# Kernel tuning notes

Hardware: AMD Instinct MI355X
Metric: run time of the kernel (lower is better)

Reference implementation:

```python
import jax, jax.numpy as jnp
import numpy as np

H, D = 16, 64  # heads, d_head
ROPE_BASE = 10000.0


def _rotate_half(x):
    # '... (d r) -> ... d r' with r=2, unbind, cat(-x2, x1)
    xs = x.reshape(*x.shape[:-1], D // 2, 2)
    x1, x2 = xs[..., 0], xs[..., 1]
    return jnp.concatenate([-x2, x1], axis=-1)


def _rope_sin_cos(n):
    inv_freq = 1.0 / (ROPE_BASE ** (jnp.arange(0, D, 2, dtype=jnp.float32) / D))  # [D/2]
    f = jnp.arange(n, dtype=jnp.float32)[:, None] * inv_freq                      # [n, D/2]
    emb = jnp.concatenate([f, f], axis=-1)                                        # [n, D]
    # cache = cat(sin(emb), cos(emb)); apply slices sin=[:D], cos=[D:]
    return jnp.sin(emb), jnp.cos(emb)


def setup_inputs() -> dict:
    key = jax.random.key(0)
    ks = jax.random.split(key, 5)
    B, N, E = 2, 2048, 1024
    C = H * D
    s = 0.02
    return {
        "x": jax.random.normal(ks[0], (B, N, E), jnp.float32),
        "Wq": jax.random.normal(ks[1], (C, E), jnp.float32) * s,
        "bq": jnp.zeros((C,), jnp.float32),
        "Wk": jax.random.normal(ks[2], (C, E), jnp.float32) * s,
        "bk": jnp.zeros((C,), jnp.float32),
        "Wv": jax.random.normal(ks[3], (C, E), jnp.float32) * s,
        "bv": jnp.zeros((C,), jnp.float32),
        "Wo": jax.random.normal(ks[4], (E, C), jnp.float32) * s,
        "bo": jnp.zeros((E,), jnp.float32),
    }


def reference(x, Wq, bq, Wk, bk, Wv, bv, Wo, bo):
    B, N, E = x.shape

    def proj(W, b):  # [B,N,E] -> [B,H,N,D]
        y = x @ W.T + b
        return y.reshape(B, N, H, D).transpose(0, 2, 1, 3)

    q, k, v = proj(Wq, bq), proj(Wk, bk), proj(Wv, bv)

    sin, cos = _rope_sin_cos(N)  # each [N, D], broadcast over [B,H,N,D]
    q = q * cos + _rotate_half(q) * sin
    k = k * cos + _rotate_half(k) * sin

    scale = 1.0 / jnp.sqrt(jnp.float32(D))
    scores = jnp.einsum('bhqd,bhkd->bhqk', q, k) * scale  # [B,H,N,N]
    causal = jnp.tril(jnp.ones((N, N), dtype=bool))
    scores = jnp.where(causal, scores, jnp.float32(-jnp.inf))
    probs = jax.nn.softmax(scores, axis=-1)
    out = jnp.einsum('bhqk,bhkd->bhqd', probs, v)
    out = out.transpose(0, 2, 1, 3).reshape(B, N, H * D)
    return out @ Wo.T + bo
```

## Files before the change

kernel.cpp:

```cpp
#include <hip/hip_runtime.h>
#include <hip/hip_bf16.h>
#include <cstdint>
#include <cstddef>

using bf16x8 = __attribute__((ext_vector_type(8))) __bf16;
using f32x4  = __attribute__((ext_vector_type(4))) float;

__device__ __forceinline__ float b2f(unsigned short u) {
  union { unsigned u; float f; } x; x.u = ((unsigned)u) << 16; return x.f;
}
__device__ __forceinline__ unsigned short f2b(float f) {
  union { float f; unsigned u; } x; x.f = f;
  unsigned r = x.u + 0x7fffu + ((x.u >> 16) & 1u);
  return (unsigned short)(r >> 16);
}
__device__ __forceinline__ unsigned short f2b_trunc(float f) {
  union { float f; unsigned u; } x; x.f = f;
  return (unsigned short)(x.u >> 16);
}

__device__ __forceinline__ void gload_lds16(const void* g, void* l) {
  __builtin_amdgcn_global_load_lds(
      (const __attribute__((address_space(1))) void*)g,
      (__attribute__((address_space(3))) void*)l, 16, 0, 0);
}

__device__ __forceinline__ bf16x8 ldfrag(const unsigned short* p) {
  return *reinterpret_cast<const bf16x8*>(p);
}

__global__ __launch_bounds__(256) void prep_kernel(const float* __restrict__ x,
                                                   const float* __restrict__ Wq,
                                                   const float* __restrict__ Wk,
                                                   const float* __restrict__ Wv,
                                                   const float* __restrict__ Wo,
                                                   unsigned short* __restrict__ xb,
                                                   unsigned short* __restrict__ wqkv,
                                                   unsigned short* __restrict__ wob,
                                                   float* __restrict__ st,
                                                   float* __restrict__ ct) {
  const int gid = blockIdx.x * 256 + threadIdx.x;
  if (gid < 65536) {
    const int n = gid >> 5, j = gid & 31;
    const float inv = powf(10000.0f, -(float)j * (1.0f / 32.0f));
    const float ang = (float)n * inv;
    st[gid] = sinf(ang);
    ct[gid] = cosf(ang);
  }
  const int XW = 1048576;
  const int WW = 262144;
#pragma unroll
  for (int it = 0; it < 4; ++it) {
    const int i = gid + it * 524288;
    const float* s; unsigned short* d; int j;
    if (i < XW)                { s = x;  d = xb;              j = i; }
    else if (i < XW + WW)      { s = Wq; d = wqkv;            j = i - XW; }
    else if (i < XW + 2 * WW)  { s = Wk; d = wqkv + 1048576;  j = i - XW - WW; }
    else if (i < XW + 3 * WW)  { s = Wv; d = wqkv + 2097152;  j = i - XW - 2 * WW; }
    else                       { s = Wo; d = wob;             j = i - XW - 3 * WW; }
    float4 v = reinterpret_cast<const float4*>(s)[j];
    ushort4 o;
    o.x = f2b(v.x); o.y = f2b(v.y); o.z = f2b(v.z); o.w = f2b(v.w);
    reinterpret_cast<ushort4*>(d)[j] = o;
  }
}

__global__ __launch_bounds__(512) void gemm256(const unsigned short* __restrict__ A,
                                               const unsigned short* __restrict__ B,
                                               unsigned short* __restrict__ Qo,
                                               unsigned short* __restrict__ Ko,
                                               unsigned short* __restrict__ Vt,
                                               const float* __restrict__ st,
                                               const float* __restrict__ ct,
                                               const float* __restrict__ bq,
                                               const float* __restrict__ bk,
                                               const float* __restrict__ bv,
                                               int M, int N, int K, int TN) {
  extern __shared__ __align__(16) unsigned short sm[];
  const int tid = threadIdx.x, lane = tid & 63, wave = tid >> 6;
  const int lr = lane & 15, lk = lane >> 4;
  const int wr = wave >> 2, wc = wave & 3;

  int wg = (int)blockIdx.x;
  const int cpx = (int)gridDim.x >> 3;
  wg = (wg & 7) * cpx + (wg >> 3);
  const int bn = (wg % TN) * 192, bm = (wg / TN) * 256;

  const int srow = wave * 8 + (lane >> 3);
  const int scol = (((lane & 7) * 16) ^ (((lane >> 3) & 7) << 4)) >> 1;
  const unsigned short* Ag = A + (size_t)(bm + srow) * K + scol;
  const unsigned short* Bg = B + (size_t)(bn + srow) * K + scol;

  auto issueA = [&](int kt, int nb, int i) {
    gload_lds16(Ag + (size_t)(i * 64) * K + (size_t)kt * 64,
                sm + nb * 28672 + wave * 512 + i * 4096);
  };
  auto issueB = [&](int kt, int nb, int i) {
    gload_lds16(Bg + (size_t)(i * 64) * K + (size_t)kt * 64,
                sm + nb * 28672 + 16384 + wave * 512 + i * 4096);
  };

  f32x4 acc[8][3] = {};
  const int swz = (lr & 7) << 4;
  const int NT = K / 64;

#pragma unroll
  for (int i = 0; i < 3; ++i) issueB(0, 0, i);
#pragma unroll
  for (int i = 0; i < 4; ++i) issueA(0, 0, i);
  asm volatile("s_waitcnt vmcnt(0)" ::: "memory");
  __builtin_amdgcn_s_barrier();

  for (int kt = 0; kt < NT; ++kt) {
    const int cur = kt & 1, nb = cur ^ 1;
    const bool pf = (kt + 1 < NT);

    const unsigned short* Ab = sm + cur * 28672 + wr * 8192;
    const unsigned short* Bb = sm + cur * 28672 + 16384;

    bf16x8 b[3][2];
#pragma unroll
    for (int n = 0; n < 3; ++n)
#pragma unroll
      for (int kk = 0; kk < 2; ++kk)
        b[n][kk] = ldfrag(&Bb[(wc * 48 + n * 16 + lr) * 64 + (((kk * 64 + lk * 16) ^ swz) >> 1)]);

#pragma unroll
    for (int q = 0; q < 4; ++q) {
      if (q == 2) {
        if (pf) asm volatile("s_waitcnt vmcnt(4)" ::: "memory");
        else    asm volatile("s_waitcnt vmcnt(0)" ::: "memory");
        __builtin_amdgcn_s_barrier();
      }
      if (pf) {
        if (q == 0)      { issueB(kt + 1, nb, 0); issueB(kt + 1, nb, 1); }
        else if (q == 1) { issueB(kt + 1, nb, 2); issueA(kt + 1, nb, 0); }
        else if (q == 2) { issueA(kt + 1, nb, 1); issueA(kt + 1, nb, 2); }
        else             { issueA(kt + 1, nb, 3); }
      }
      bf16x8 a[2][2];
#pragma unroll
      for (int m = 0; m < 2; ++m)
#pragma unroll
        for (int kk = 0; kk < 2; ++kk)
          a[m][kk] = ldfrag(&Ab[((q * 2 + m) * 16 + lr) * 64 + (((kk * 64 + lk * 16) ^ swz) >> 1)]);
      __builtin_amdgcn_s_barrier();
      __builtin_amdgcn_s_setprio(1);
#pragma unroll
      for (int kk = 0; kk < 2; ++kk)
#pragma unroll
        for (int m = 0; m < 2; ++m)
#pragma unroll
          for (int n = 0; n < 3; ++n)
            acc[q * 2 + m][n] =
                __builtin_amdgcn_mfma_f32_16x16x32_bf16(a[m][kk], b[n][kk], acc[q * 2 + m][n], 0, 0, 0);
      __builtin_amdgcn_s_setprio(0);
      if (q < 3) __builtin_amdgcn_s_barrier();
    }

    if (pf) {
      asm volatile("s_waitcnt vmcnt(1)" ::: "memory");
      __builtin_amdgcn_s_barrier();
    }
  }

  __syncthreads();

  const int btok = bm >> 11;
  const int ntok0 = bm & 2047;

#pragma unroll
  for (int n = 0; n < 3; ++n) {
    const int col = bn + wc * 48 + n * 16 + lr;
    if (col >= 2048) {
      const int vcol = col - 2048;
      const float bvv = bv[vcol];
      const int h = vcol >> 6, d = vcol & 63;
      unsigned short* vrow = Vt + ((size_t)((btok * 16 + h) * 64 + d)) * 2048;
#pragma unroll
      for (int mu = 0; mu < 4; ++mu) {
        uint4 w;
        w.x = (unsigned)f2b(acc[2 * mu][n][0] + bvv)     | ((unsigned)f2b(acc[2 * mu][n][1] + bvv) << 16);
        w.y = (unsigned)f2b(acc[2 * mu][n][2] + bvv)     | ((unsigned)f2b(acc[2 * mu][n][3] + bvv) << 16);
        w.z = (unsigned)f2b(acc[2 * mu + 1][n][0] + bvv) | ((unsigned)f2b(acc[2 * mu + 1][n][1] + bvv) << 16);
        w.w = (unsigned)f2b(acc[2 * mu + 1][n][2] + bvv) | ((unsigned)f2b(acc[2 * mu + 1][n][3] + bvv) << 16);
        const int ncol = ntok0 + wr * 128 + mu * 32 + 8 * lk;
        *reinterpret_cast<uint4*>(vrow + ncol) = w;
      }
    } else {
      const float bvv = (col < 1024) ? bq[col] : bk[col & 1023];
      const int lcol = wc * 48 + n * 16 + lr;
#pragma unroll
      for (int m = 0; m < 8; ++m)
#pragma unroll
        for (int r = 0; r < 4; ++r) {
          const int lrow = wr * 128 + m * 16 + lk * 4 + r;
          const int g2 = (lcol >> 3) ^ (lrow & 7);
          sm[lrow * 192 + (g2 << 3) + (lcol & 7)] = f2b(acc[m][n][r] + bvv);
        }
    }
  }
  __syncthreads();

  const int nqk = min(3, max(0, (2048 - bn) >> 6));
  for (int t = tid; t < 256 * nqk; t += 512) {
    const int hh = t >> 8, row = t & 255;
    const int ntok = ntok0 + row;
    const int col0 = bn + hh * 64;
    const bool isq = col0 < 1024;
    const int h = (col0 & 1023) >> 6;
    const float* ctp = ct + ntok * 32;
    const float* stp = st + ntok * 32;
    unsigned short xr[64];
#pragma unroll
    for (int i = 0; i < 8; ++i) {
      const int g = (hh * 8 + i) ^ (row & 7);
      *reinterpret_cast<int4*>(&xr[i * 8]) =
          *reinterpret_cast<const int4*>(&sm[row * 192 + g * 8]);
    }
    unsigned short out[64];
#pragma unroll
    for (int i = 0; i < 32; ++i) {
      const float c = ctp[i], s = stp[i];
      float o1 = b2f(xr[i]) * c - b2f(xr[2 * i + 1]) * s;
      float o2 = b2f(xr[32 + i]) * c + b2f(xr[2 * i]) * s;
      if (isq) { o1 *= 0.18033688f; o2 *= 0.18033688f; }
      out[i] = f2b(o1);
      out[32 + i] = f2b(o2);
    }
    unsigned short* dst =
        (isq ? Qo : Ko) + ((size_t)((btok * 16 + h) * 2048 + ntok)) * 64;
#pragma unroll
    for (int i = 0; i < 8; ++i)
      *reinterpret_cast<int4*>(dst + i * 8) =
          *reinterpret_cast<const int4*>(&out[i * 8]);
  }
}

template <int OUTF32>
__global__ __launch_bounds__(256) void gemm_bt(const unsigned short* __restrict__ A,
                                               const unsigned short* __restrict__ B,
                                               void* __restrict__ C,
                                               const float* __restrict__ bias,
                                               int M, int N, int K) {
  __shared__ __align__(16) unsigned short As[128 * 32];
  __shared__ __align__(16) unsigned short Bs[128 * 32];
  const int tid = threadIdx.x;
  const int lane = tid & 63, wave = tid >> 6;
  const int wr = wave >> 1, wc = wave & 1;
  const int bm = blockIdx.y * 128, bn = blockIdx.x * 128;
  const int lr = lane & 15, lk = lane >> 4;
  f32x4 acc[4][4] = {};

  for (int k0 = 0; k0 < K; k0 += 32) {
#pragma unroll
    for (int i = 0; i < 2; ++i) {
      int idx = i * 256 + tid;
      int row = idx >> 2, c8 = (idx & 3) * 8;
      gload_lds16(A + (size_t)(bm + row) * K + k0 + c8, &As[(i * 256 + wave * 64) * 8]);
      gload_lds16(B + (size_t)(bn + row) * K + k0 + c8, &Bs[(i * 256 + wave * 64) * 8]);
    }
    __syncthreads();
    bf16x8 af[4], bfr[4];
#pragma unroll
    for (int mi = 0; mi < 4; ++mi)
      af[mi] = ldfrag(&As[(wr * 64 + mi * 16 + lr) * 32 + lk * 8]);
#pragma unroll
    for (int ni = 0; ni < 4; ++ni)
      bfr[ni] = ldfrag(&Bs[(wc * 64 + ni * 16 + lr) * 32 + lk * 8]);
#pragma unroll
    for (int mi = 0; mi < 4; ++mi)
#pragma unroll
      for (int ni = 0; ni < 4; ++ni)
        acc[mi][ni] = __builtin_amdgcn_mfma_f32_16x16x32_bf16(af[mi], bfr[ni], acc[mi][ni], 0, 0, 0);
    __syncthreads();
  }

#pragma unroll
  for (int mi = 0; mi < 4; ++mi) {
#pragma unroll
    for (int ni = 0; ni < 4; ++ni) {
      int col = bn + wc * 64 + ni * 16 + lr;
      float bv = bias ? bias[col] : 0.0f;
#pragma unroll
      for (int r = 0; r < 4; ++r) {
        int row = bm + wr * 64 + mi * 16 + lk * 4 + r;
        float v = acc[mi][ni][r] + bv;
        if (OUTF32)
          reinterpret_cast<float*>(C)[(size_t)row * N + col] = v;
        else
          reinterpret_cast<unsigned short*>(C)[(size_t)row * N + col] = f2b(v);
      }
    }
  }
}

__global__ __launch_bounds__(512) void flash_kernel(const unsigned short* __restrict__ Q,
                                                    const unsigned short* __restrict__ Kb,
                                                    const unsigned short* __restrict__ Vt,
                                                    unsigned short* __restrict__ Out, int N) {
  extern __shared__ __align__(16) unsigned short smem[];
  unsigned short* KsB = smem;
  unsigned short* VsB = smem + 16384;

  const int tid = threadIdx.x;
  const int lane = tid & 63, wave = tid >> 6;
  const int lr = lane & 15, lk = lane >> 4;
  const int bh = blockIdx.x;
  const int x = blockIdx.y;
  const int qtA = x, qtB = 15 - x;
  const int ntA = x + 1;
  const unsigned short* Qh = Q + (size_t)bh * N * 64;
  const unsigned short* Kh = Kb + (size_t)bh * N * 64;
  const unsigned short* Vh = Vt + (size_t)bh * 64 * N;

  const int wrowA = qtA * 128 + wave * 16;
  const int wrowB = qtB * 128 + wave * 16;

  const int kr = tid >> 3;
  const int kcb = ((tid & 7) * 16) ^ ((kr & 7) << 4);
  const unsigned short* Kg0 = Kh + (size_t)kr * 64 + (kcb >> 1);
  const int vr = tid >> 4;
  const int vcb = ((tid & 15) * 16) ^ ((vr & 7) << 4);
  const unsigned short* Vg0 = Vh + (size_t)vr * N + (vcb >> 1);

  auto stage = [&](int buf, int tk) {
    const unsigned short* kp = Kg0 + (size_t)tk * 8192;
    const unsigned short* vp = Vg0 + (size_t)tk * 128;
    unsigned short* kl = KsB + buf * 8192 + wave * 512;
    unsigned short* vl = VsB + buf * 8192 + wave * 512;
    gload_lds16(kp, kl);
    gload_lds16(kp + 4096, kl + 4096);
    gload_lds16(vp, vl);
    gload_lds16(vp + (size_t)32 * N, vl + 4096);
  };

  stage(0, 0);

  bf16x8 qA0 = ldfrag(&Qh[(size_t)(wrowA + lr) * 64 + lk * 8]);
  bf16x8 qA1 = ldfrag(&Qh[(size_t)(wrowA + lr) * 64 + 32 + lk * 8]);
  bf16x8 qB0 = ldfrag(&Qh[(size_t)(wrowB + lr) * 64 + lk * 8]);
  bf16x8 qB1 = ldfrag(&Qh[(size_t)(wrowB + lr) * 64 + 32 + lk * 8]);

  bf16x8 ones;
  {
    union { unsigned short u; __bf16 b; } one; one.u = 0x3F80;
#pragma unroll
    for (int j = 0; j < 8; ++j) ones[j] = one.b;
  }

  const float NEG = -1e30f;
  f32x4 oacc[4] = {};
  f32x4 lacc = {};
  float m_run = NEG;

  auto compute_phase = [&](int buf, bf16x8 q0, bf16x8 q1, bool diag) {
    const unsigned short* Ksb = KsB + buf * 8192;
    const unsigned short* Vsb = VsB + buf * 8192;
    f32x4 s[8];
#pragma unroll
    for (int ni = 0; ni < 8; ++ni) s[ni] = f32x4{0.f, 0.f, 0.f, 0.f};
    __builtin_amdgcn_s_setprio(1);
#pragma unroll
    for (int ni = 0; ni < 8; ++ni) {
      const int R = ni * 16 + lr;
      const int sw = (R & 7) << 4;
      bf16x8 kf0 = ldfrag(&Ksb[R * 64 + (((lk * 16) ^ sw) >> 1)]);
      bf16x8 kf1 = ldfrag(&Ksb[R * 64 + (((64 + lk * 16) ^ sw) >> 1)]);
      s[ni] = __builtin_amdgcn_mfma_f32_16x16x32_bf16(kf0, q0, s[ni], 0, 0, 0);
      s[ni] = __builtin_amdgcn_mfma_f32_16x16x32_bf16(kf1, q1, s[ni], 0, 0, 0);
    }
    __builtin_amdgcn_s_setprio(0);

    if (diag) {
      const int ql = wave * 16 + lr;
#pragma unroll
      for (int ni = 0; ni < 8; ++ni)
#pragma unroll
        for (int r = 0; r < 4; ++r)
          if (ni * 16 + lk * 4 + r > ql) s[ni][r] = NEG;
    }

    float mx = s[0][0];
#pragma unroll
    for (int ni = 0; ni < 8; ++ni)
#pragma unroll
      for (int r = 0; r < 4; ++r)
        if (ni || r) mx = fmaxf(mx, s[ni][r]);
    mx = fmaxf(mx, __shfl_xor(mx, 16, 64));
    mx = fmaxf(mx, __shfl_xor(mx, 32, 64));

    if (!__all(mx - m_run <= 8.0f)) {
      float nm = fmaxf(m_run, mx);
      float alpha = __builtin_amdgcn_exp2f(m_run - nm);
      m_run = nm;
#pragma unroll
      for (int ni = 0; ni < 4; ++ni) oacc[ni] *= alpha;
      lacc *= alpha;
    }

    unsigned pk[8][2];
#pragma unroll
    for (int ni = 0; ni < 8; ++ni) {
      float p0 = __builtin_amdgcn_exp2f(s[ni][0] - m_run);
      float p1 = __builtin_amdgcn_exp2f(s[ni][1] - m_run);
      float p2 = __builtin_amdgcn_exp2f(s[ni][2] - m_run);
      float p3 = __builtin_amdgcn_exp2f(s[ni][3] - m_run);
      pk[ni][0] = (unsigned)f2b_trunc(p0) | ((unsigned)f2b_trunc(p1) << 16);
      pk[ni][1] = (unsigned)f2b_trunc(p2) | ((unsigned)f2b_trunc(p3) << 16);
    }

    __builtin_amdgcn_s_setprio(1);
#pragma unroll
    for (int c = 0; c < 4; ++c) {
      union { unsigned u[4]; bf16x8 v; } pb;
      pb.u[0] = pk[2 * c][0];
      pb.u[1] = pk[2 * c][1];
      pb.u[2] = pk[2 * c + 1][0];
      pb.u[3] = pk[2 * c + 1][1];
      lacc = __builtin_amdgcn_mfma_f32_16x16x32_bf16(ones, pb.v, lacc, 0, 0, 0);
      const int cb = c * 64 + lk * 16;
#pragma unroll
      for (int ni = 0; ni < 4; ++ni) {
        const int RV = ni * 16 + lr;
        bf16x8 vf = ldfrag(&Vsb[RV * 128 + ((cb ^ ((RV & 7) << 4)) >> 1)]);
        oacc[ni] = __builtin_amdgcn_mfma_f32_16x16x32_bf16(vf, pb.v, oacc[ni], 0, 0, 0);
      }
    }
    __builtin_amdgcn_s_setprio(0);
  };

  const int b = bh >> 4, h = bh & 15;
  auto epilogue = [&](int wrow0) {
    const float rl = 1.0f / lacc[0];
    const int q = wrow0 + lr;
#pragma unroll
    for (int ni = 0; ni < 4; ++ni) {
      uint2 w;
      w.x = (unsigned)f2b(oacc[ni][0] * rl) | ((unsigned)f2b(oacc[ni][1] * rl) << 16);
      w.y = (unsigned)f2b(oacc[ni][2] * rl) | ((unsigned)f2b(oacc[ni][3] * rl) << 16);
      *reinterpret_cast<uint2*>(
          &Out[((size_t)(b * N + q)) * 1024 + h * 64 + ni * 16 + lk * 4]) = w;
    }
  };

  __syncthreads();

  int buf = 0;
  for (int p = 0; p < 17; ++p) {
    if (p + 1 < 17) {
      int tk2 = (p + 1 < ntA) ? (p + 1) : (p + 1 - ntA);
      stage(buf ^ 1, tk2);
    }
    if (p == ntA) {
      epilogue(wrowA);
#pragma unroll
      for (int ni = 0; ni < 4; ++ni) oacc[ni] = f32x4{0.f, 0.f, 0.f, 0.f};
      lacc = f32x4{0.f, 0.f, 0.f, 0.f};
      m_run = NEG;
    }
    if (p < ntA) compute_phase(buf, qA0, qA1, p == ntA - 1);
    else         compute_phase(buf, qB0, qB1, p == 16);
    __syncthreads();
    buf ^= 1;
  }
  epilogue(wrowB);
}

extern "C" void kernel_launch(void* const* d_in, const int* in_sizes, int n_in,
                              void* d_out, int out_size, void* d_ws, size_t ws_size,
                              hipStream_t stream) {
  const int B = 2, N = 2048, E = 1024, C = 1024, NC = 3072;
  const int M = B * N;

  const float* x  = (const float*)d_in[0];
  const float* Wq = (const float*)d_in[1];
  const float* bq = (const float*)d_in[2];
  const float* Wk = (const float*)d_in[3];
  const float* bk = (const float*)d_in[4];
  const float* Wv = (const float*)d_in[5];
  const float* bv = (const float*)d_in[6];
  const float* Wo = (const float*)d_in[7];
  const float* bo = (const float*)d_in[8];

  char* w = (char*)d_ws;
  size_t off = 0;
  auto alloc = [&](size_t bytes) {
    void* p = w + off;
    off += (bytes + 255) & ~(size_t)255;
    return p;
  };
  unsigned short* xb    = (unsigned short*)alloc((size_t)M * E * 2);
  unsigned short* wqkv  = (unsigned short*)alloc((size_t)NC * E * 2);
  unsigned short* wob   = (unsigned short*)alloc((size_t)E * C * 2);
  unsigned short* qb    = (unsigned short*)alloc((size_t)B * 16 * N * 64 * 2);
  unsigned short* kb    = (unsigned short*)alloc((size_t)B * 16 * N * 64 * 2);
  unsigned short* vt    = (unsigned short*)alloc((size_t)B * 16 * 64 * N * 2);
  unsigned short* attnb = (unsigned short*)alloc((size_t)M * C * 2);
  float* sin_t = (float*)alloc((size_t)N * 32 * 4);
  float* cos_t = (float*)alloc((size_t)N * 32 * 4);

  prep_kernel<<<2048, 256, 0, stream>>>(x, Wq, Wk, Wv, Wo, xb, wqkv, wob, sin_t, cos_t);

  static const int GEMM_LDS = 114688;
  hipFuncSetAttribute(reinterpret_cast<const void*>(gemm256),
                      hipFuncAttributeMaxDynamicSharedMemorySize, GEMM_LDS);
  gemm256<<<dim3((NC / 192) * (M / 256)), 512, GEMM_LDS, stream>>>(
      xb, wqkv, qb, kb, vt, sin_t, cos_t, bq, bk, bv, M, NC, E, NC / 192);

  static const int FLASH_LDS = 65536;
  hipFuncSetAttribute(reinterpret_cast<const void*>(flash_kernel),
                      hipFuncAttributeMaxDynamicSharedMemorySize, FLASH_LDS);
  flash_kernel<<<dim3(B * 16, 8), 512, FLASH_LDS, stream>>>(qb, kb, vt, attnb, N);

  gemm_bt<1><<<dim3(E / 128, M / 128), 256, 0, stream>>>(attnb, wob, d_out, bo, M, E, C);
}
```

Before: 109.9 us.

## Double-buffer output projection GEMM with swizzled LDS and BK=64

Replaces the simple single-buffered output-projection GEMM with a version that prefetches the next 64-wide K tile into a second LDS buffer while computing the current one. It adds an XOR swizzle to the LDS layout to reduce bank conflicts on fragment loads, and raises wave priority around the MFMA bursts. This aims to hide global load latency and halve the barrier count per K. In exchange it uses 64KB of dynamic LDS, which may reduce occupancy.

```diff
diff --git a/kernel.cpp b/kernel.cpp
--- a/kernel.cpp
+++ b/kernel.cpp
@@ -237,59 +237,87 @@
   }
 }
 
-template <int OUTF32>
-__global__ __launch_bounds__(256) void gemm_bt(const unsigned short* __restrict__ A,
-                                               const unsigned short* __restrict__ B,
-                                               void* __restrict__ C,
-                                               const float* __restrict__ bias,
-                                               int M, int N, int K) {
-  __shared__ __align__(16) unsigned short As[128 * 32];
-  __shared__ __align__(16) unsigned short Bs[128 * 32];
-  const int tid = threadIdx.x;
-  const int lane = tid & 63, wave = tid >> 6;
+__global__ __launch_bounds__(256) void gemm_out(const unsigned short* __restrict__ A,
+                                                const unsigned short* __restrict__ B,
+                                                float* __restrict__ C,
+                                                const float* __restrict__ bias,
+                                                int M, int N, int K) {
+  extern __shared__ __align__(16) unsigned short sm[];
+  const int tid = threadIdx.x, lane = tid & 63, wave = tid >> 6;
+  const int lr = lane & 15, lk = lane >> 4;
   const int wr = wave >> 1, wc = wave & 1;
   const int bm = blockIdx.y * 128, bn = blockIdx.x * 128;
-  const int lr = lane & 15, lk = lane >> 4;
+
+  const int srow = tid >> 3;
+  const int scol = (((tid & 7) * 16) ^ ((srow & 7) << 4)) >> 1;
+  const unsigned short* Ag = A + (size_t)(bm + srow) * K + scol;
+  const unsigned short* Bg = B + (size_t)(bn + srow) * K + scol;
+
+  auto stage = [&](int kt, int nb) {
+    const size_t ko = (size_t)kt * 64;
+    unsigned short* base = sm + nb * 16384 + wave * 512;
+#pragma unroll
+    for (int i = 0; i < 4; ++i)
+      gload_lds16(Ag + (size_t)(i * 32) * K + ko, base + i * 2048);
+#pragma unroll
+    for (int i = 0; i < 4; ++i)
+      gload_lds16(Bg + (size_t)(i * 32) * K + ko, base + 8192 + i * 2048);
+  };
+
   f32x4 acc[4][4] = {};
-
-  for (int k0 = 0; k0 < K; k0 += 32) {
-#pragma unroll
-    for (int i = 0; i < 2; ++i) {
-      int idx = i * 256 + tid;
-      int row = idx >> 2, c8 = (idx & 3) * 8;
-      gload_lds16(A + (size_t)(bm + row) * K + k0 + c8, &As[(i * 256 + wave * 64) * 8]);
-      gload_lds16(B + (size_t)(bn + row) * K + k0 + c8, &Bs[(i * 256 + wave * 64) * 8]);
-    }
-    __syncthreads();
-    bf16x8 af[4], bfr[4];
-#pragma unroll
-    for (int mi = 0; mi < 4; ++mi)
-      af[mi] = ldfrag(&As[(wr * 64 + mi * 16 + lr) * 32 + lk * 8]);
-#pragma unroll
-    for (int ni = 0; ni < 4; ++ni)
-      bfr[ni] = ldfrag(&Bs[(wc * 64 + ni * 16 + lr) * 32 + lk * 8]);
-#pragma unroll
-    for (int mi = 0; mi < 4; ++mi)
-#pragma unroll
-      for (int ni = 0; ni < 4; ++ni)
-        acc[mi][ni] = __builtin_amdgcn_mfma_f32_16x16x32_bf16(af[mi], bfr[ni], acc[mi][ni], 0, 0, 0);
-    __syncthreads();
-  }
-
-#pragma unroll
-  for (int mi = 0; mi < 4; ++mi) {
-#pragma unroll
-    for (int ni = 0; ni < 4; ++ni) {
-      int col = bn + wc * 64 + ni * 16 + lr;
-      float bv = bias ? bias[col] : 0.0f;
+  const int swz = (lr & 7) << 4;
+  const int NT = K / 64;
+
+  stage(0, 0);
+  asm volatile("s_waitcnt vmcnt(0)" ::: "memory");
+  __builtin_amdgcn_s_barrier();
+
+  for (int kt = 0; kt < NT; ++kt) {
+    const int cur = kt & 1;
+    const bool pf = (kt + 1 < NT);
+    if (pf) stage(kt + 1, cur ^ 1);
+
+    const unsigned short* Ab = sm + cur * 16384 + (size_t)wr * 64 * 64;
+    const unsigned short* Bb = sm + cur * 16384 + 8192 + (size_t)wc * 64 * 64;
+
+    bf16x8 b[4][2];
+#pragma unroll
+    for (int n = 0; n < 4; ++n)
+#pragma unroll
+      for (int kk = 0; kk < 2; ++kk)
+        b[n][kk] = ldfrag(&Bb[(n * 16 + lr) * 64 + (((kk * 64 + lk * 16) ^ swz) >> 1)]);
+
+#pragma unroll
+    for (int m = 0; m < 4; ++m) {
+      bf16x8 a[2];
+#pragma unroll
+      for (int kk = 0; kk < 2; ++kk)
+        a[kk] = ldfrag(&Ab[(m * 16 + lr) * 64 + (((kk * 64 + lk * 16) ^ swz) >> 1)]);
+      __builtin_amdgcn_s_setprio(1);
+#pragma unroll
+      for (int kk = 0; kk < 2; ++kk)
+#pragma unroll
+        for (int n = 0; n < 4; ++n)
+          acc[m][n] = __builtin_amdgcn_mfma_f32_16x16x32_bf16(a[kk], b[n][kk], acc[m][n], 0, 0, 0);
+      __builtin_amdgcn_s_setprio(0);
+    }
+
+    if (pf) {
+      asm volatile("s_waitcnt vmcnt(0)" ::: "memory");
+      __builtin_amdgcn_s_barrier();
+    }
+  }
+
+#pragma unroll
+  for (int m = 0; m < 4; ++m) {
+#pragma unroll
+    for (int n = 0; n < 4; ++n) {
+      const int col = bn + wc * 64 + n * 16 + lr;
+      const float bvv = bias[col];
 #pragma unroll
       for (int r = 0; r < 4; ++r) {
-        int row = bm + wr * 64 + mi * 16 + lk * 4 + r;
-        float v = acc[mi][ni][r] + bv;
-        if (OUTF32)
-          reinterpret_cast<float*>(C)[(size_t)row * N + col] = v;
-        else
-          reinterpret_cast<unsigned short*>(C)[(size_t)row * N + col] = f2b(v);
+        const int row = bm + wr * 64 + m * 16 + lk * 4 + r;
+        C[(size_t)row * N + col] = acc[m][n][r] + bvv;
       }
     }
   }
@@ -513,5 +541,9 @@
                       hipFuncAttributeMaxDynamicSharedMemorySize, FLASH_LDS);
   flash_kernel<<<dim3(B * 16, 8), 512, FLASH_LDS, stream>>>(qb, kb, vt, attnb, N);
 
-  gemm_bt<1><<<dim3(E / 128, M / 128), 256, 0, stream>>>(attnb, wob, d_out, bo, M, E, C);
-}
+  static const int OUT_LDS = 65536;
+  hipFuncSetAttribute(reinterpret_cast<const void*>(gemm_out),
+                      hipFuncAttributeMaxDynamicSharedMemorySize, OUT_LDS);
+  gemm_out<<<dim3(E / 128, M / 128), 256, OUT_LDS, stream>>>(
+      attnb, wob, (float*)d_out, bo, M, E, C);
+}
```

New measurement: 99.34 us. -9.6%, faster.
